# Kernel optimization log

Hardware: AMD Instinct MI355X
Metric: run time of the kernel (lower is better)

Reference implementation:

```python
import jax, jax.numpy as jnp
import numpy as np

D = 2048  # dims
T = 8192  # sequence length


def _layernorm(x, g, b):
    m = jnp.mean(x, axis=-1, keepdims=True)
    v = jnp.mean(jnp.square(x - m), axis=-1, keepdims=True)
    return (x - m) * jax.lax.rsqrt(v + 1e-5) * g + b


def _lerp(a, b, t):
    # torch.lerp(a, b, t) = a + t*(b-a)
    return a + t * (b - a)


def _wkv(k, v, time_first, time_decay):
    """RWKV power-decay attention (numerically stable scan).
    k, v: [T, D]. w = -exp(time_decay) is the per-channel log-decay."""
    u = time_first
    w = -jnp.exp(time_decay)

    def step(carry, kv):
        aa, bb, pp = carry  # running num, den, max-exponent, each [D]
        kt, vt = kv
        ww = u + kt
        p = jnp.maximum(pp, ww)
        e1 = jnp.exp(pp - p)
        e2 = jnp.exp(ww - p)
        out = (e1 * aa + e2 * vt) / (e1 * bb + e2)
        ww2 = pp + w
        p2 = jnp.maximum(ww2, kt)
        e1 = jnp.exp(ww2 - p2)
        e2 = jnp.exp(kt - p2)
        return (e1 * aa + e2 * vt, e1 * bb + e2, p2), out

    init = (jnp.zeros((D,), k.dtype), jnp.zeros((D,), k.dtype),
            jnp.full((D,), -1e38, k.dtype))
    _, out = jax.lax.scan(step, init, (k, v))
    return out  # [T, D]


def setup_inputs() -> dict:
    key = jax.random.key(0)
    ks = iter(jax.random.split(key, 40))
    s = 1.0 / np.sqrt(D)
    inp = {"x": jax.random.normal(next(ks), (T, D), jnp.float32)}
    for name in ["attk", "attv", "attr", "atto", "ffnk", "ffnv", "ffnr"]:
        inp[name + "_w"] = jax.random.normal(next(ks), (D, D), jnp.float32) * s
        inp[name + "_b"] = jax.random.normal(next(ks), (D,), jnp.float32) * 0.02
    inp["ln1_g"] = jnp.ones((D,), jnp.float32)
    inp["ln1_b"] = jnp.zeros((D,), jnp.float32)
    inp["ln2_g"] = jnp.ones((D,), jnp.float32)
    inp["ln2_b"] = jnp.zeros((D,), jnp.float32)
    for name in ["attmixk", "attmixv", "attmixr", "ffnmixk", "ffnmixr"]:
        inp[name] = jax.random.uniform(next(ks), (D,), jnp.float32)
    inp["time_first"] = jax.random.normal(next(ks), (D,), jnp.float32) * 0.1
    inp["time_decay"] = jax.random.normal(next(ks), (D,), jnp.float32) * 0.1
    return inp


def reference(x, attk_w, attk_b, attv_w, attv_b, attr_w, attr_b, atto_w, atto_b,
              ffnk_w, ffnk_b, ffnv_w, ffnv_b, ffnr_w, ffnr_b,
              ln1_g, ln1_b, ln2_g, ln2_b,
              attmixk, attmixv, attmixr, ffnmixk, ffnmixr,
              time_first, time_decay):
    # --- time-mix (attention) branch ---
    xy = _layernorm(x, ln1_g, ln1_b)
    tc = jnp.roll(xy, 1, axis=0)  # token shift
    k = _lerp(tc, xy, attmixk) @ attk_w.T + attk_b
    v = _lerp(tc, xy, attmixv) @ attv_w.T + attv_b
    r = jax.nn.sigmoid(_lerp(tc, xy, attmixr) @ attr_w.T + attr_b)
    wkv = _wkv(k, v, time_first, time_decay) * r
    rz = x + wkv @ atto_w.T + atto_b
    # --- channel-mix (FFN) branch ---
    ddd = _layernorm(rz, ln2_g, ln2_b)
    rc = jnp.roll(ddd, 1, axis=0)
    rf = jax.nn.sigmoid(_lerp(rc, ddd, ffnmixr) @ ffnr_w.T + ffnr_b)
    kf = jax.nn.relu(_lerp(rc, ddd, ffnmixk) @ ffnk_w.T + ffnk_b)
    rvm = jnp.square(kf) @ ffnv_w.T + ffnv_b
    return rvm * rf + rz
```

## Files before the change

### kernel.cpp

```cpp
#include <hip/hip_runtime.h>
#include <cstdint>
#include <cstddef>


#define SEQ 8192
#define DIM 2048
#define NCH 128
#define CL  64

typedef unsigned short u16;
typedef __attribute__((ext_vector_type(8))) short bf16x8;
typedef __attribute__((ext_vector_type(4))) float f32x4;

__device__ __forceinline__ u16 f2bf(float f) {
  unsigned x = __float_as_uint(f);
  x += 0x7fffu + ((x >> 16) & 1u);
  return (u16)(x >> 16);
}
__device__ __forceinline__ float bf2f(u16 h) {
  return __uint_as_float((unsigned)h << 16);
}

__global__ void __launch_bounds__(256) convert_weights(
    const float* w0, const float* w1, const float* w2, const float* w3,
    const float* w4, const float* w5, const float* w6, u16* dst)
{
  const float* s;
  switch (blockIdx.y) {
    case 0: s = w0; break; case 1: s = w1; break; case 2: s = w2; break;
    case 3: s = w3; break; case 4: s = w4; break; case 5: s = w5; break;
    default: s = w6; break;
  }
  size_t i = ((size_t)blockIdx.x * 256 + threadIdx.x) * 4;
  float4 f = *(const float4*)(s + i);
  *(ushort4*)(dst + (size_t)blockIdx.y * DIM * DIM + i) =
      make_ushort4(f2bf(f.x), f2bf(f.y), f2bf(f.z), f2bf(f.w));
}

__device__ __forceinline__ void store_mix8(u16* dst, const float* mix,
                                           const float* yc, const float* yp)
{
  float4 ma = *(const float4*)(mix);
  float4 mb = *(const float4*)(mix + 4);
  float mv[8] = {ma.x, ma.y, ma.z, ma.w, mb.x, mb.y, mb.z, mb.w};
  u16 uu[8];
  #pragma unroll
  for (int j = 0; j < 8; ++j)
    uu[j] = f2bf(yp[j] + mv[j] * (yc[j] - yp[j]));
  *(ushort4*)dst       = make_ushort4(uu[0], uu[1], uu[2], uu[3]);
  *(ushort4*)(dst + 4) = make_ushort4(uu[4], uu[5], uu[6], uu[7]);
}

template<int NOUT>
__global__ void __launch_bounds__(256) ln_mix_kernel(
    const float* __restrict__ X, const float* __restrict__ gw, const float* __restrict__ bw,
    const float* __restrict__ mix0, const float* __restrict__ mix1, const float* __restrict__ mix2,
    u16* __restrict__ o0, u16* __restrict__ o1, u16* __restrict__ o2)
{
  const int t  = blockIdx.x;
  const int tp = (t == 0) ? (SEQ - 1) : (t - 1);
  const int tid = threadIdx.x, lane = tid & 63, wid = tid >> 6;
  const int base = tid * 8;
  const float* xc = X + (size_t)t  * DIM + base;
  const float* xp = X + (size_t)tp * DIM + base;
  float4 ca = *(const float4*)xc, cb2 = *(const float4*)(xc + 4);
  float4 pa = *(const float4*)xp, pb2 = *(const float4*)(xp + 4);
  float cv[8] = {ca.x, ca.y, ca.z, ca.w, cb2.x, cb2.y, cb2.z, cb2.w};
  float pv[8] = {pa.x, pa.y, pa.z, pa.w, pb2.x, pb2.y, pb2.z, pb2.w};
  float4 s = {0.f, 0.f, 0.f, 0.f};
  #pragma unroll
  for (int j = 0; j < 8; ++j) {
    s.x += cv[j]; s.y += cv[j] * cv[j];
    s.z += pv[j]; s.w += pv[j] * pv[j];
  }
  #pragma unroll
  for (int off = 32; off > 0; off >>= 1) {
    s.x += __shfl_down(s.x, off);
    s.y += __shfl_down(s.y, off);
    s.z += __shfl_down(s.z, off);
    s.w += __shfl_down(s.w, off);
  }
  __shared__ float4 wred[4];
  if (lane == 0) wred[wid] = s;
  __syncthreads();
  float4 tt;
  tt.x = wred[0].x + wred[1].x + wred[2].x + wred[3].x;
  tt.y = wred[0].y + wred[1].y + wred[2].y + wred[3].y;
  tt.z = wred[0].z + wred[1].z + wred[2].z + wred[3].z;
  tt.w = wred[0].w + wred[1].w + wred[2].w + wred[3].w;
  constexpr float inv = 1.0f / DIM;
  const float mc = tt.x * inv, vc = tt.y * inv - mc * mc;
  const float rc = 1.0f / sqrtf(vc + 1e-5f);
  const float mp = tt.z * inv, vp = tt.w * inv - mp * mp;
  const float rp = 1.0f / sqrtf(vp + 1e-5f);
  float4 ga = *(const float4*)(gw + base), gb = *(const float4*)(gw + base + 4);
  float4 ba = *(const float4*)(bw + base), bb = *(const float4*)(bw + base + 4);
  float gv[8] = {ga.x, ga.y, ga.z, ga.w, gb.x, gb.y, gb.z, gb.w};
  float bv[8] = {ba.x, ba.y, ba.z, ba.w, bb.x, bb.y, bb.z, bb.w};
  float yc[8], yp[8];
  #pragma unroll
  for (int j = 0; j < 8; ++j) {
    yc[j] = (cv[j] - mc) * rc * gv[j] + bv[j];
    yp[j] = (pv[j] - mp) * rp * gv[j] + bv[j];
  }
  store_mix8(o0 + (size_t)t * DIM + base, mix0 + base, yc, yp);
  store_mix8(o1 + (size_t)t * DIM + base, mix1 + base, yc, yp);
  if constexpr (NOUT == 3)
    store_mix8(o2 + (size_t)t * DIM + base, mix2 + base, yc, yp);
}

template<int EPI>
__global__ void __launch_bounds__(256) gemm_bt(
    const u16* __restrict__ A, const u16* __restrict__ B,
    const float* __restrict__ bias,
    const float* __restrict__ exf, const u16* __restrict__ exb,
    float* __restrict__ Cf, u16* __restrict__ Cb)
{
  constexpr int BK = 32;
  __shared__ u16 As[128 * BK];
  __shared__ u16 Bs[128 * BK];
  const int tid  = threadIdx.x;
  const int lane = tid & 63;
  const int wid  = tid >> 6;
  const int wr = wid >> 1, wc = wid & 1;
  const int tm = blockIdx.y * 128, tn = blockIdx.x * 128;
  const int frow = lane & 15, fko = (lane >> 4) * 8;
  const int cb = wid * 2;
  f32x4 acc[4][4] = {};

  for (int k0 = 0; k0 < DIM; k0 += BK) {
    __syncthreads();
    #pragma unroll
    for (int j = 0; j < 2; ++j) {
      const int chunk = (cb + j) * 64 + lane;
      const int row = chunk >> 2;
      const int c8  = (chunk & 3) * 8;
      const u16* ga = A + (size_t)(tm + row) * DIM + k0 + c8;
      const u16* gb = B + (size_t)(tn + row) * DIM + k0 + c8;
      __builtin_amdgcn_global_load_lds(
          (const __attribute__((address_space(1))) void*)ga,
          (__attribute__((address_space(3))) void*)(As + (cb + j) * 512), 16, 0, 0);
      __builtin_amdgcn_global_load_lds(
          (const __attribute__((address_space(1))) void*)gb,
          (__attribute__((address_space(3))) void*)(Bs + (cb + j) * 512), 16, 0, 0);
    }
    __syncthreads();
    bf16x8 af[4], bf[4];
    #pragma unroll
    for (int m = 0; m < 4; ++m)
      af[m] = *(const bf16x8*)(As + (wr * 64 + m * 16 + frow) * BK + fko);
    #pragma unroll
    for (int n = 0; n < 4; ++n)
      bf[n] = *(const bf16x8*)(Bs + (wc * 64 + n * 16 + frow) * BK + fko);
    #pragma unroll
    for (int m = 0; m < 4; ++m)
      #pragma unroll
      for (int n = 0; n < 4; ++n)
        acc[m][n] = __builtin_amdgcn_mfma_f32_16x16x32_bf16(af[m], bf[n], acc[m][n], 0, 0, 0);
  }

  #pragma unroll
  for (int n = 0; n < 4; ++n) {
    const int cn = tn + wc * 64 + n * 16 + frow;
    const float bv = bias[cn];
    #pragma unroll
    for (int m = 0; m < 4; ++m) {
      const int r0 = tm + wr * 64 + m * 16 + (lane >> 4) * 4;
      #pragma unroll
      for (int i = 0; i < 4; ++i) {
        const size_t idx = (size_t)(r0 + i) * DIM + cn;
        float val = acc[m][n][i] + bv;
        if constexpr (EPI == 0)      { Cb[idx] = f2bf(val); }
        else if constexpr (EPI == 1) { Cb[idx] = f2bf(1.0f / (1.0f + __expf(-val))); }
        else if constexpr (EPI == 2) { Cf[idx] = val + exf[idx]; }
        else if constexpr (EPI == 3) { float r = fmaxf(val, 0.0f); Cb[idx] = f2bf(r * r); }
        else                         { Cf[idx] = val * bf2f(exb[idx]) + exf[idx]; }
      }
    }
  }
}

__global__ void __launch_bounds__(256) wkv_phase1(
    const u16* __restrict__ k, const u16* __restrict__ v,
    const float* __restrict__ tdec,
    float* __restrict__ Sa, float* __restrict__ Sb, float* __restrict__ Sp)
{
  const int d = blockIdx.y * 256 + threadIdx.x;
  const int c = blockIdx.x;
  const float w = -__expf(tdec[d]);
  float aa = 0.f, bb = 0.f, pp = -1e38f;
  const int t0 = c * CL;
  for (int t = t0; t < t0 + CL; ++t) {
    const size_t idx = (size_t)t * DIM + d;
    const float kk = bf2f(k[idx]), vv = bf2f(v[idx]);
    const float ww2 = pp + w;
    const float p2 = fmaxf(ww2, kk);
    const float e1 = __expf(ww2 - p2), e2 = __expf(kk - p2);
    aa = e1 * aa + e2 * vv;
    bb = e1 * bb + e2;
    pp = p2;
  }
  Sa[(size_t)c * DIM + d] = aa;
  Sb[(size_t)c * DIM + d] = bb;
  Sp[(size_t)c * DIM + d] = pp;
}

__global__ void __launch_bounds__(256) wkv_phase2(
    const float* __restrict__ Sa, const float* __restrict__ Sb, const float* __restrict__ Sp,
    const float* __restrict__ tdec,
    float* __restrict__ Pa, float* __restrict__ Pb, float* __restrict__ Pp)
{
  const int d = blockIdx.x * 256 + threadIdx.x;
  const float w = -__expf(tdec[d]);
  const float Lw = (float)CL * w;
  float aa = 0.f, bb = 0.f, pp = -1e38f;
  for (int c = 0; c < NCH; ++c) {
    const size_t idx = (size_t)c * DIM + d;
    Pa[idx] = aa; Pb[idx] = bb; Pp[idx] = pp;
    const float dp = pp + Lw;
    const float sa = Sa[idx], sb = Sb[idx], sp = Sp[idx];
    const float p = fmaxf(dp, sp);
    const float e1 = __expf(dp - p), e2 = __expf(sp - p);
    aa = e1 * aa + e2 * sa;
    bb = e1 * bb + e2 * sb;
    pp = p;
  }
}

__global__ void __launch_bounds__(256) wkv_phase3(
    const u16* __restrict__ k, const u16* __restrict__ v, const u16* __restrict__ r,
    const float* __restrict__ Pa, const float* __restrict__ Pb, const float* __restrict__ Pp,
    const float* __restrict__ tfirst, const float* __restrict__ tdec,
    u16* __restrict__ outb)
{
  const int d = blockIdx.y * 256 + threadIdx.x;
  const int c = blockIdx.x;
  const float u = tfirst[d];
  const float w = -__expf(tdec[d]);
  const size_t sidx = (size_t)c * DIM + d;
  float aa = Pa[sidx], bb = Pb[sidx], pp = Pp[sidx];
  const int t0 = c * CL;
  for (int t = t0; t < t0 + CL; ++t) {
    const size_t idx = (size_t)t * DIM + d;
    const float kk = bf2f(k[idx]), vv = bf2f(v[idx]);
    const float ww = u + kk;
    const float p = fmaxf(pp, ww);
    float e1 = __expf(pp - p), e2 = __expf(ww - p);
    const float out = (e1 * aa + e2 * vv) / (e1 * bb + e2);
    outb[idx] = f2bf(out * bf2f(r[idx]));
    const float ww2 = pp + w;
    const float p2 = fmaxf(ww2, kk);
    e1 = __expf(ww2 - p2); e2 = __expf(kk - p2);
    aa = e1 * aa + e2 * vv;
    bb = e1 * bb + e2;
    pp = p2;
  }
}

extern "C" void kernel_launch(void* const* d_in, const int* in_sizes, int n_in,
                              void* d_out, int out_size, void* d_ws, size_t ws_size,
                              hipStream_t stream)
{
  const float* x      = (const float*)d_in[0];
  const float* attk_w = (const float*)d_in[1];
  const float* attk_b = (const float*)d_in[2];
  const float* attv_w = (const float*)d_in[3];
  const float* attv_b = (const float*)d_in[4];
  const float* attr_w = (const float*)d_in[5];
  const float* attr_b = (const float*)d_in[6];
  const float* atto_w = (const float*)d_in[7];
  const float* atto_b = (const float*)d_in[8];
  const float* ffnk_w = (const float*)d_in[9];
  const float* ffnk_b = (const float*)d_in[10];
  const float* ffnv_w = (const float*)d_in[11];
  const float* ffnv_b = (const float*)d_in[12];
  const float* ffnr_w = (const float*)d_in[13];
  const float* ffnr_b = (const float*)d_in[14];
  const float* ln1_g  = (const float*)d_in[15];
  const float* ln1_b  = (const float*)d_in[16];
  const float* ln2_g  = (const float*)d_in[17];
  const float* ln2_b  = (const float*)d_in[18];
  const float* amixk  = (const float*)d_in[19];
  const float* amixv  = (const float*)d_in[20];
  const float* amixr  = (const float*)d_in[21];
  const float* fmixk  = (const float*)d_in[22];
  const float* fmixr  = (const float*)d_in[23];
  const float* tfirst = (const float*)d_in[24];
  const float* tdecay = (const float*)d_in[25];
  float* out = (float*)d_out;

  const size_t WE = (size_t)DIM * DIM;
  const size_t SD = (size_t)SEQ * DIM;
  u16* Wbf = (u16*)d_ws;
  u16* xk  = Wbf + 7 * WE;
  u16* xv  = xk + SD;
  u16* xr  = xv + SD;
  u16* kb  = xr + SD;
  u16* vb  = kb + SD;
  u16* rb  = vb + SD;
  float* Sa = (float*)(rb + SD);
  float* Sb = Sa + (size_t)NCH * DIM;
  float* Sp = Sb + (size_t)NCH * DIM;
  float* Pa = Sp + (size_t)NCH * DIM;
  float* Pb = Pa + (size_t)NCH * DIM;
  float* Pp = Pb + (size_t)NCH * DIM;
  u16*   wkvr = xk;
  float* rz   = (float*)xv;
  u16*   xkf  = kb;
  u16*   xrf  = vb;
  u16*   rf   = rb;
  u16*   kf2  = xk;

  const dim3 gg(DIM / 128, SEQ / 128);
  const dim3 gwkv(NCH, DIM / 256);

  convert_weights<<<dim3(DIM * DIM / 1024, 7), 256, 0, stream>>>(
      attk_w, attv_w, attr_w, atto_w, ffnk_w, ffnv_w, ffnr_w, Wbf);

  ln_mix_kernel<3><<<SEQ, 256, 0, stream>>>(x, ln1_g, ln1_b, amixk, amixv, amixr, xk, xv, xr);
  gemm_bt<0><<<gg, 256, 0, stream>>>(xk, Wbf + 0 * WE, attk_b, nullptr, nullptr, nullptr, kb);
  gemm_bt<0><<<gg, 256, 0, stream>>>(xv, Wbf + 1 * WE, attv_b, nullptr, nullptr, nullptr, vb);
  gemm_bt<1><<<gg, 256, 0, stream>>>(xr, Wbf + 2 * WE, attr_b, nullptr, nullptr, nullptr, rb);
  wkv_phase1<<<gwkv, 256, 0, stream>>>(kb, vb, tdecay, Sa, Sb, Sp);
  wkv_phase2<<<DIM / 256, 256, 0, stream>>>(Sa, Sb, Sp, tdecay, Pa, Pb, Pp);
  wkv_phase3<<<gwkv, 256, 0, stream>>>(kb, vb, rb, Pa, Pb, Pp, tfirst, tdecay, wkvr);
  gemm_bt<2><<<gg, 256, 0, stream>>>(wkvr, Wbf + 3 * WE, atto_b, x, nullptr, rz, nullptr);

  ln_mix_kernel<2><<<SEQ, 256, 0, stream>>>(rz, ln2_g, ln2_b, fmixk, fmixr, nullptr, xkf, xrf, nullptr);
  gemm_bt<1><<<gg, 256, 0, stream>>>(xrf, Wbf + 6 * WE, ffnr_b, nullptr, nullptr, nullptr, rf);
  gemm_bt<3><<<gg, 256, 0, stream>>>(xkf, Wbf + 4 * WE, ffnk_b, nullptr, nullptr, nullptr, kf2);
  gemm_bt<4><<<gg, 256, 0, stream>>>(kf2, Wbf + 5 * WE, ffnv_b, rz, rf, out, nullptr);
}
```

Before: 1.149 ms.

## Double-buffer GEMM LDS tiles and swizzle block order for L2 reuse

The bf16 GEMM now uses two LDS buffers, so the async global-to-LDS load of the next K tile is issued before the MFMAs on the current tile run. This overlaps memory latency with compute and cuts barriers per tile from two to one. Block indices are remapped so consecutive blocks share B column tiles across eight groups, which should improve L2 locality. It also adds a min-occupancy launch bound of 4, and doubles LDS use. The swizzle hardcodes a grid of 16 column tiles by 64 row tiles.

```diff
diff --git a/kernel.cpp b/kernel.cpp
--- a/kernel.cpp
+++ b/kernel.cpp
@@ -110,54 +110,78 @@
 }
 
 template<int EPI>
-__global__ void __launch_bounds__(256) gemm_bt(
+__global__ void __launch_bounds__(256, 4) gemm_bt(
     const u16* __restrict__ A, const u16* __restrict__ B,
     const float* __restrict__ bias,
     const float* __restrict__ exf, const u16* __restrict__ exb,
     float* __restrict__ Cf, u16* __restrict__ Cb)
 {
   constexpr int BK = 32;
-  __shared__ u16 As[128 * BK];
-  __shared__ u16 Bs[128 * BK];
+  constexpr int NT = DIM / BK;
+  __shared__ u16 As[2][128 * BK];
+  __shared__ u16 Bs[2][128 * BK];
   const int tid  = threadIdx.x;
   const int lane = tid & 63;
   const int wid  = tid >> 6;
   const int wr = wid >> 1, wc = wid & 1;
-  const int tm = blockIdx.y * 128, tn = blockIdx.x * 128;
+  const int bid = blockIdx.y * gridDim.x + blockIdx.x;
+  const int nb  = (bid & 7) * 128 + (bid >> 3);
+  const int tn  = (nb & 15) * 128;
+  const int tm  = (nb >> 4) * 128;
   const int frow = lane & 15, fko = (lane >> 4) * 8;
   const int cb = wid * 2;
   f32x4 acc[4][4] = {};
 
-  for (int k0 = 0; k0 < DIM; k0 += BK) {
+#define GSTAGE(b, k0)                                                           \
+  {                                                                             \
+    _Pragma("unroll")                                                           \
+    for (int j = 0; j < 2; ++j) {                                               \
+      const int chunk = (cb + j) * 64 + lane;                                   \
+      const int row = chunk >> 2;                                               \
+      const int c8  = (chunk & 3) * 8;                                          \
+      const u16* ga = A + (size_t)(tm + row) * DIM + (k0) + c8;                 \
+      const u16* gb = B + (size_t)(tn + row) * DIM + (k0) + c8;                 \
+      __builtin_amdgcn_global_load_lds(                                         \
+          (const __attribute__((address_space(1))) void*)ga,                    \
+          (__attribute__((address_space(3))) void*)(&As[b][0] + (cb + j) * 512),\
+          16, 0, 0);                                                            \
+      __builtin_amdgcn_global_load_lds(                                         \
+          (const __attribute__((address_space(1))) void*)gb,                    \
+          (__attribute__((address_space(3))) void*)(&Bs[b][0] + (cb + j) * 512),\
+          16, 0, 0);                                                            \
+    }                                                                           \
+  }
+
+#define GCOMPUTE(b)                                                             \
+  {                                                                             \
+    bf16x8 af[4], bfr[4];                                                       \
+    _Pragma("unroll")                                                           \
+    for (int m = 0; m < 4; ++m)                                                 \
+      af[m] = *(const bf16x8*)(&As[b][0] + (wr * 64 + m * 16 + frow) * BK + fko);\
+    _Pragma("unroll")                                                           \
+    for (int n = 0; n < 4; ++n)                                                 \
+      bfr[n] = *(const bf16x8*)(&Bs[b][0] + (wc * 64 + n * 16 + frow) * BK + fko);\
+    _Pragma("unroll")                                                           \
+    for (int m = 0; m < 4; ++m)                                                 \
+      _Pragma("unroll")                                                         \
+      for (int n = 0; n < 4; ++n)                                               \
+        acc[m][n] = __builtin_amdgcn_mfma_f32_16x16x32_bf16(af[m], bfr[n],      \
+                                                            acc[m][n], 0, 0, 0);\
+  }
+
+  GSTAGE(0, 0);
+  __syncthreads();
+  #pragma unroll 1
+  for (int t = 0; t < NT; t += 2) {
+    GSTAGE(1, (t + 1) * BK);
+    GCOMPUTE(0);
     __syncthreads();
-    #pragma unroll
-    for (int j = 0; j < 2; ++j) {
-      const int chunk = (cb + j) * 64 + lane;
-      const int row = chunk >> 2;
-      const int c8  = (chunk & 3) * 8;
-      const u16* ga = A + (size_t)(tm + row) * DIM + k0 + c8;
-      const u16* gb = B + (size_t)(tn + row) * DIM + k0 + c8;
-      __builtin_amdgcn_global_load_lds(
-          (const __attribute__((address_space(1))) void*)ga,
-          (__attribute__((address_space(3))) void*)(As + (cb + j) * 512), 16, 0, 0);
-      __builtin_amdgcn_global_load_lds(
-          (const __attribute__((address_space(1))) void*)gb,
-          (__attribute__((address_space(3))) void*)(Bs + (cb + j) * 512), 16, 0, 0);
-    }
+    if (t + 2 < NT) GSTAGE(0, (t + 2) * BK);
+    GCOMPUTE(1);
     __syncthreads();
-    bf16x8 af[4], bf[4];
-    #pragma unroll
-    for (int m = 0; m < 4; ++m)
-      af[m] = *(const bf16x8*)(As + (wr * 64 + m * 16 + frow) * BK + fko);
-    #pragma unroll
-    for (int n = 0; n < 4; ++n)
-      bf[n] = *(const bf16x8*)(Bs + (wc * 64 + n * 16 + frow) * BK + fko);
-    #pragma unroll
-    for (int m = 0; m < 4; ++m)
-      #pragma unroll
-      for (int n = 0; n < 4; ++n)
-        acc[m][n] = __builtin_amdgcn_mfma_f32_16x16x32_bf16(af[m], bf[n], acc[m][n], 0, 0, 0);
-  }
+  }
+#undef GSTAGE
+#undef GCOMPUTE
 
   #pragma unroll
   for (int n = 0; n < 4; ++n) {
```

After: 1.006 ms. 1.14x faster.
